# Optimization experiments

Measured on AMD Instinct MI355X. Metric: run time of the kernel, lower is better.

The kernel has to match this reference:

```python
import jax, jax.numpy as jnp
import numpy as np

FEAT_SIZE, HIDDEN_SIZE, ATT_SIZE = 2048, 1024, 512
BATCH, FEAT_NUM = 64, 512


def setup_inputs() -> dict:
    key = jax.random.key(0)
    ks = jax.random.split(key, 8)
    s = lambda fan_in: 1.0 / np.sqrt(fan_in)
    return {
        "feats": jax.random.normal(ks[0], (BATCH, FEAT_NUM, FEAT_SIZE), jnp.float32),
        "key": jax.random.normal(ks[1], (BATCH, HIDDEN_SIZE), jnp.float32),
        "wh_w": jax.random.uniform(ks[2], (ATT_SIZE, HIDDEN_SIZE), jnp.float32, -s(HIDDEN_SIZE), s(HIDDEN_SIZE)),
        "wh_b": jax.random.uniform(ks[3], (ATT_SIZE,), jnp.float32, -s(HIDDEN_SIZE), s(HIDDEN_SIZE)),
        "wv_w": jax.random.uniform(ks[4], (ATT_SIZE, FEAT_SIZE), jnp.float32, -s(FEAT_SIZE), s(FEAT_SIZE)),
        "wv_b": jax.random.uniform(ks[5], (ATT_SIZE,), jnp.float32, -s(FEAT_SIZE), s(FEAT_SIZE)),
        "wa_w": jax.random.uniform(ks[6], (1, ATT_SIZE), jnp.float32, -s(ATT_SIZE), s(ATT_SIZE)),
    }


def reference(feats, key, wh_w, wh_b, wv_w, wv_b, wa_w):
    # v = wv(feats): (B, N, A)
    v = jnp.einsum('bnf,af->bna', feats, wv_w) + wv_b
    # h = wh(key): (B, A), broadcast-added over feat_num
    h = key @ wh_w.T + wh_b
    inputs = h[:, None, :] + v                       # (B, N, A)
    scores = jnp.einsum('bna,a->bn', jnp.tanh(inputs), wa_w[0])  # (B, N)
    alpha = jax.nn.softmax(scores, axis=1)           # (B, N)
    att_feats = jnp.einsum('bn,bnf->bf', alpha, feats)  # (B, F)
    return (att_feats, alpha)
```

## Files before the change

kernel.cpp:

```cpp
#include <hip/hip_runtime.h>
#include <hip/hip_bf16.h>

#define FEATSZ 2048
#define HIDSZ  1024
#define ATTSZ  512
#define BATCH  64
#define FEATN  512

typedef float  f32x4  __attribute__((ext_vector_type(4)));
typedef __bf16 bf16x8 __attribute__((ext_vector_type(8)));

__device__ __forceinline__ unsigned short f2bf(float f) {
    union { float f; unsigned int u; } x; x.f = f;
    unsigned int u = x.u;
    return (unsigned short)((u + 0x7fffu + ((u >> 16) & 1u)) >> 16);
}

__global__ void k_h(const float* __restrict__ key, const float* __restrict__ wh_w,
                    const float* __restrict__ wh_b, float* __restrict__ h) {
    const int b = blockIdx.y;
    const int ac = blockIdx.x;
    const int t = threadIdx.x;
    const int lane = t & 63, wv = t >> 6;
    float k16[16];
    const float* kb = key + b * HIDSZ;
#pragma unroll
    for (int j = 0; j < 16; ++j) k16[j] = kb[lane + 64 * j];
#pragma unroll 1
    for (int i = 0; i < 16; ++i) {
        int a = ac * 64 + wv * 16 + i;
        const float* wr = wh_w + (size_t)a * HIDSZ;
        float s = 0.f;
#pragma unroll
        for (int j = 0; j < 16; ++j) s += k16[j] * wr[lane + 64 * j];
#pragma unroll
        for (int d = 32; d; d >>= 1) s += __shfl_xor(s, d);
        if (lane == 0) h[b * ATTSZ + a] = s + wh_b[a];
    }
}

__global__ void k_wvcvt(const float* __restrict__ wv_w, unsigned short* __restrict__ wvb) {
    int idx = blockIdx.x * 256 + threadIdx.x;
    int a = idx >> 11, k = idx & 2047;
    int CF = a >> 4, c = a & 15, ks = k >> 5, kin = k & 31;
    int lane = c + ((kin >> 3) << 4);
    int dst = ((ks * 32 + CF) * 64 + lane) * 8 + (kin & 7);
    wvb[dst] = f2bf(wv_w[idx]);
}

__global__ __launch_bounds__(256, 4) void k_scores(
        const float* __restrict__ feats, const unsigned short* __restrict__ wvb,
        const float* __restrict__ h, const float* __restrict__ wv_b,
        const float* __restrict__ wa, float* __restrict__ part_sc) {
    __shared__ __align__(16) char smem[40960];

    const int t = threadIdx.x, lane = t & 63, w = t >> 6;
    const int wm = w >> 1, wn = w & 1;
    const int xcd = blockIdx.x & 7, idx = blockIdx.x >> 3;
    const int mb = xcd * 32 + (idx >> 2);
    const int nc = idx & 3;
    const int m0 = mb * 128, b = mb >> 2;

    auto Abuf = [&](int i) -> char* { return smem + i * 8192; };
    auto Bbuf = [&](int i) -> char* { return smem + 16384 + i * 8192; };

    const int sr = t >> 1, shf = t & 1;
    const float* gA = feats + (size_t)(m0 + sr) * FEATSZ + shf * 16;
    const int sx = (sr >> 1) & 3;
    const int wof0 = sr * 64 + (((shf * 2    ) ^ sx) * 16);
    const int wof1 = sr * 64 + (((shf * 2 + 1) ^ sx) * 16);

    const char* gBb = (const char*)wvb + (size_t)(nc * 8) * 1024 + (size_t)(w * 2) * 1024 + lane * 16;
    const int bdst = (w * 2) * 1024;

    const int l15 = lane & 15;
    const int abase = (wm * 64 + l15) * 64 + (((lane >> 4) ^ ((l15 >> 1) & 3)) * 16);
    const int bbase = (wn * 4) * 1024 + lane * 16;

    f32x4 acc[4][4];
#pragma unroll
    for (int m = 0; m < 4; ++m)
#pragma unroll
        for (int cf = 0; cf < 4; ++cf) acc[m][cf] = (f32x4)0.0f;

    f32x4 GA0, GA1, GA2, GA3;

    auto gloadB = [&](char* dst, int kk) {
#pragma unroll
        for (int i = 0; i < 2; ++i)
            __builtin_amdgcn_global_load_lds(
                (const __attribute__((address_space(1))) void*)(gBb + (size_t)kk * 32768 + i * 1024),
                (__attribute__((address_space(3))) void*)(dst + bdst + i * 1024),
                16, 0, 0);
    };
    auto ldGA = [&](int kk) {
        const float* p = gA + kk * 32;
        GA0 = *(const f32x4*)p;       GA1 = *(const f32x4*)(p + 4);
        GA2 = *(const f32x4*)(p + 8); GA3 = *(const f32x4*)(p + 12);
    };
    auto cvtWrite = [&](char* dst) {
        bf16x8 v0, v1;
        v0[0] = (__bf16)GA0[0]; v0[1] = (__bf16)GA0[1]; v0[2] = (__bf16)GA0[2]; v0[3] = (__bf16)GA0[3];
        v0[4] = (__bf16)GA1[0]; v0[5] = (__bf16)GA1[1]; v0[6] = (__bf16)GA1[2]; v0[7] = (__bf16)GA1[3];
        v1[0] = (__bf16)GA2[0]; v1[1] = (__bf16)GA2[1]; v1[2] = (__bf16)GA2[2]; v1[3] = (__bf16)GA2[3];
        v1[4] = (__bf16)GA3[0]; v1[5] = (__bf16)GA3[1]; v1[6] = (__bf16)GA3[2]; v1[7] = (__bf16)GA3[3];
        *(bf16x8*)__builtin_assume_aligned(dst + wof0, 16) = v0;
        *(bf16x8*)__builtin_assume_aligned(dst + wof1, 16) = v1;
    };

    ldGA(0);
    gloadB(Bbuf(0), 0);
    gloadB(Bbuf(1), 1);
    cvtWrite(Abuf(0));
    ldGA(1);
    asm volatile("s_waitcnt vmcnt(6)" ::: "memory");
    asm volatile("s_waitcnt lgkmcnt(0)" ::: "memory");
    __builtin_amdgcn_s_barrier();
    __builtin_amdgcn_sched_barrier(0);

#pragma unroll 1
    for (int j = 0; j < 64; ++j) {
        const char* ar = Abuf(j & 1);
        char*       aw = Abuf((j & 1) ^ 1);
        const char* br = Bbuf(j % 3);
        if (j < 62) gloadB(Bbuf((j + 2) % 3), j + 2);
        bf16x8 BF[4], AF[4];
#pragma unroll
        for (int cf = 0; cf < 4; ++cf)
            BF[cf] = *(const bf16x8*)__builtin_assume_aligned(br + bbase + cf * 1024, 16);
#pragma unroll
        for (int m = 0; m < 4; ++m)
            AF[m] = *(const bf16x8*)__builtin_assume_aligned(ar + abase + m * 1024, 16);
        __builtin_amdgcn_s_setprio(1);
#pragma unroll
        for (int m = 0; m < 4; ++m)
#pragma unroll
            for (int cf = 0; cf < 4; ++cf)
                acc[m][cf] = __builtin_amdgcn_mfma_f32_16x16x32_bf16(AF[m], BF[cf], acc[m][cf], 0, 0, 0);
        __builtin_amdgcn_s_setprio(0);
        if (j < 63) cvtWrite(aw);
        if (j < 62) ldGA(j + 2);
        if (j < 62) asm volatile("s_waitcnt vmcnt(6)" ::: "memory");
        else        asm volatile("s_waitcnt vmcnt(0)" ::: "memory");
        asm volatile("s_waitcnt lgkmcnt(0)" ::: "memory");
        __builtin_amdgcn_s_barrier();
        __builtin_amdgcn_sched_barrier(0);
    }

    const int c16 = lane & 15, q4 = lane >> 4;
    float hreg[4], wreg[4];
#pragma unroll
    for (int cf = 0; cf < 4; ++cf) {
        int a = nc * 128 + wn * 64 + cf * 16 + c16;
        hreg[cf] = h[b * ATTSZ + a] + wv_b[a];
        wreg[cf] = wa[a];
    }
    float pv[4][4];
#pragma unroll
    for (int m = 0; m < 4; ++m)
#pragma unroll
        for (int jr = 0; jr < 4; ++jr) pv[m][jr] = 0.f;
#pragma unroll
    for (int m = 0; m < 4; ++m)
#pragma unroll
        for (int cf = 0; cf < 4; ++cf)
#pragma unroll
            for (int jr = 0; jr < 4; ++jr)
                pv[m][jr] += tanhf(acc[m][cf][jr] + hreg[cf]) * wreg[cf];
#pragma unroll
    for (int m = 0; m < 4; ++m)
#pragma unroll
        for (int jr = 0; jr < 4; ++jr) {
            float v = pv[m][jr];
            v += __shfl_xor(v, 1); v += __shfl_xor(v, 2);
            v += __shfl_xor(v, 4); v += __shfl_xor(v, 8);
            pv[m][jr] = v;
        }
    float* scp = (float*)smem;
    __builtin_amdgcn_s_barrier();
    if (c16 == 0) {
#pragma unroll
        for (int m = 0; m < 4; ++m)
#pragma unroll
            for (int jr = 0; jr < 4; ++jr)
                scp[wn * 128 + wm * 64 + m * 16 + q4 * 4 + jr] = pv[m][jr];
    }
    __syncthreads();
    if (t < 128)
        part_sc[(size_t)nc * (BATCH * FEATN) + m0 + t] = scp[t] + scp[128 + t];
}

__global__ void k_softmax(const float* __restrict__ part_sc, float* __restrict__ alpha) {
    __shared__ float red[16];
    const int b = blockIdx.x, t = threadIdx.x;
    const int lane = t & 63, w = t >> 6;
    const int r = b * FEATN + t;
    float s = part_sc[r] + part_sc[BATCH * FEATN + r]
            + part_sc[2 * BATCH * FEATN + r] + part_sc[3 * BATCH * FEATN + r];
    float m = s;
#pragma unroll
    for (int d = 32; d; d >>= 1) m = fmaxf(m, __shfl_xor(m, d));
    if (lane == 0) red[w] = m;
    __syncthreads();
    if (t == 0) {
        float mm = red[0];
        for (int i = 1; i < 8; ++i) mm = fmaxf(mm, red[i]);
        red[8] = mm;
    }
    __syncthreads();
    float e = __expf(s - red[8]);
    float sum = e;
#pragma unroll
    for (int d = 32; d; d >>= 1) sum += __shfl_xor(sum, d);
    if (lane == 0) red[w] = sum;
    __syncthreads();
    if (t == 0) {
        float ss = 0.f;
        for (int i = 0; i < 8; ++i) ss += red[i];
        red[9] = 1.0f / ss;
    }
    __syncthreads();
    alpha[b * FEATN + t] = e * red[9];
}

__global__ void k_att_part(const float* __restrict__ feats, const float* __restrict__ alpha,
                           float* __restrict__ part) {
    const int b = blockIdx.x, fc = blockIdx.y, ns = blockIdx.z, t = threadIdx.x;
    const int f0 = fc * 1024 + t * 4;
    const float* fp = feats + (size_t)(b * FEATN + ns * 128) * FEATSZ + f0;
    const float* al = alpha + b * FEATN + ns * 128;
    float4 acc = {0.f, 0.f, 0.f, 0.f};
#pragma unroll 4
    for (int i = 0; i < 128; ++i) {
        float a = al[i];
        float4 v = *(const float4*)(fp + (size_t)i * FEATSZ);
        acc.x += a * v.x; acc.y += a * v.y; acc.z += a * v.z; acc.w += a * v.w;
    }
    *(float4*)(part + ((size_t)ns * BATCH + b) * FEATSZ + f0) = acc;
}

__global__ void k_att_red(const float* __restrict__ part, float* __restrict__ out) {
    const int idx = (blockIdx.x * 256 + threadIdx.x) * 4;
    float4 s = *(const float4*)(part + idx);
#pragma unroll
    for (int z = 1; z < 4; ++z) {
        float4 v = *(const float4*)(part + (size_t)z * (BATCH * FEATSZ) + idx);
        s.x += v.x; s.y += v.y; s.z += v.z; s.w += v.w;
    }
    *(float4*)(out + idx) = s;
}

extern "C" void kernel_launch(void* const* d_in, const int* in_sizes, int n_in,
                              void* d_out, int out_size, void* d_ws, size_t ws_size,
                              hipStream_t stream) {
    const float* feats = (const float*)d_in[0];
    const float* key   = (const float*)d_in[1];
    const float* wh_w  = (const float*)d_in[2];
    const float* wh_b  = (const float*)d_in[3];
    const float* wv_w  = (const float*)d_in[4];
    const float* wv_b  = (const float*)d_in[5];
    const float* wa_w  = (const float*)d_in[6];

    float* out_att   = (float*)d_out;
    float* out_alpha = out_att + BATCH * FEATSZ;

    char* ws = (char*)d_ws;
    float* h            = (float*)(ws);
    float* part_sc      = (float*)(ws + 131072);
    unsigned short* wvb = (unsigned short*)(ws + 655360);
    float* part         = (float*)(ws + 655360);

    hipLaunchKernelGGL(k_h,        dim3(8, 64),    dim3(256), 0, stream, key, wh_w, wh_b, h);
    hipLaunchKernelGGL(k_wvcvt,    dim3(4096),     dim3(256), 0, stream, wv_w, wvb);
    hipLaunchKernelGGL(k_scores,   dim3(1024),     dim3(256), 0, stream, feats, wvb, h, wv_b, wa_w, part_sc);
    hipLaunchKernelGGL(k_softmax,  dim3(64),       dim3(512), 0, stream, part_sc, out_alpha);
    hipLaunchKernelGGL(k_att_part, dim3(64, 2, 4), dim3(256), 0, stream, feats, out_alpha, part);
    hipLaunchKernelGGL(k_att_red,  dim3(128),      dim3(256), 0, stream, part, out_att);
}
```

Measured before the change: 184.7 us.

## Double K-step per iteration in scores GEMM to halve barriers

The scores GEMM main loop now processes a K-chunk of 64 per iteration instead of 32, with two MFMA sub-steps per barrier. The feats staging loads 32 floats per thread, and the LDS swizzle is widened to 128-byte rows. Wv is double-buffered instead of triple-buffered, and LDS per block grows to 64KB with the occupancy hint removed. The aim is to halve the barrier and waitcnt count per unit of work, at the cost of fewer resident blocks per CU and a shallower B prefetch.

```diff
diff --git a/kernel.cpp b/kernel.cpp
--- a/kernel.cpp
+++ b/kernel.cpp
@@ -48,11 +48,11 @@
     wvb[dst] = f2bf(wv_w[idx]);
 }
 
-__global__ __launch_bounds__(256, 4) void k_scores(
+__global__ __launch_bounds__(256) void k_scores(
         const float* __restrict__ feats, const unsigned short* __restrict__ wvb,
         const float* __restrict__ h, const float* __restrict__ wv_b,
         const float* __restrict__ wa, float* __restrict__ part_sc) {
-    __shared__ __align__(16) char smem[40960];
+    __shared__ __align__(16) char smem[65536];
 
     const int t = threadIdx.x, lane = t & 63, w = t >> 6;
     const int wm = w >> 1, wn = w & 1;
@@ -61,20 +61,27 @@
     const int nc = idx & 3;
     const int m0 = mb * 128, b = mb >> 2;
 
-    auto Abuf = [&](int i) -> char* { return smem + i * 8192; };
-    auto Bbuf = [&](int i) -> char* { return smem + 16384 + i * 8192; };
+    auto Abuf = [&](int i) -> char* { return smem + i * 16384; };
+    auto Bbuf = [&](int i) -> char* { return smem + 32768 + i * 16384; };
 
     const int sr = t >> 1, shf = t & 1;
-    const float* gA = feats + (size_t)(m0 + sr) * FEATSZ + shf * 16;
-    const int sx = (sr >> 1) & 3;
-    const int wof0 = sr * 64 + (((shf * 2    ) ^ sx) * 16);
-    const int wof1 = sr * 64 + (((shf * 2 + 1) ^ sx) * 16);
-
-    const char* gBb = (const char*)wvb + (size_t)(nc * 8) * 1024 + (size_t)(w * 2) * 1024 + lane * 16;
-    const int bdst = (w * 2) * 1024;
-
-    const int l15 = lane & 15;
-    const int abase = (wm * 64 + l15) * 64 + (((lane >> 4) ^ ((l15 >> 1) & 3)) * 16);
+    const float* gA = feats + (size_t)(m0 + sr) * FEATSZ + shf * 32;
+    int wof[4];
+#pragma unroll
+    for (int q = 0; q < 4; ++q)
+        wof[q] = sr * 128 + (((shf * 4 + q) ^ (sr & 7)) * 16);
+
+    const char* wvbb = (const char*)wvb;
+    unsigned int bsrc[4];
+#pragma unroll
+    for (int i = 0; i < 4; ++i) {
+        int c = w * 4 + i;
+        bsrc[i] = (unsigned int)(((c >> 3) * 32 + nc * 8 + (c & 7)) * 1024 + lane * 16);
+    }
+    const int bdst0 = (w * 4) * 1024 + lane * 16;
+
+    const int l15 = lane & 15, aq = lane >> 4, ax = lane & 7;
+    const int arow = (wm * 64 + l15) * 128;
     const int bbase = (wn * 4) * 1024 + lane * 16;
 
     f32x4 acc[4][4];
@@ -83,65 +90,76 @@
 #pragma unroll
         for (int cf = 0; cf < 4; ++cf) acc[m][cf] = (f32x4)0.0f;
 
-    f32x4 GA0, GA1, GA2, GA3;
-
-    auto gloadB = [&](char* dst, int kk) {
-#pragma unroll
-        for (int i = 0; i < 2; ++i)
+    f32x4 GA0, GA1, GA2, GA3, GA4, GA5, GA6, GA7;
+
+    auto gloadB = [&](char* dst, int j) {
+#pragma unroll
+        for (int i = 0; i < 4; ++i)
             __builtin_amdgcn_global_load_lds(
-                (const __attribute__((address_space(1))) void*)(gBb + (size_t)kk * 32768 + i * 1024),
-                (__attribute__((address_space(3))) void*)(dst + bdst + i * 1024),
+                (const __attribute__((address_space(1))) void*)(wvbb + (size_t)j * 65536 + bsrc[i]),
+                (__attribute__((address_space(3))) void*)(dst + bdst0 + i * 1024),
                 16, 0, 0);
     };
-    auto ldGA = [&](int kk) {
-        const float* p = gA + kk * 32;
-        GA0 = *(const f32x4*)p;       GA1 = *(const f32x4*)(p + 4);
-        GA2 = *(const f32x4*)(p + 8); GA3 = *(const f32x4*)(p + 12);
+    auto ldGA = [&](int j) {
+        const float* p = gA + j * 64;
+        GA0 = *(const f32x4*)(p);      GA1 = *(const f32x4*)(p + 4);
+        GA2 = *(const f32x4*)(p + 8);  GA3 = *(const f32x4*)(p + 12);
+        GA4 = *(const f32x4*)(p + 16); GA5 = *(const f32x4*)(p + 20);
+        GA6 = *(const f32x4*)(p + 24); GA7 = *(const f32x4*)(p + 28);
     };
     auto cvtWrite = [&](char* dst) {
-        bf16x8 v0, v1;
-        v0[0] = (__bf16)GA0[0]; v0[1] = (__bf16)GA0[1]; v0[2] = (__bf16)GA0[2]; v0[3] = (__bf16)GA0[3];
-        v0[4] = (__bf16)GA1[0]; v0[5] = (__bf16)GA1[1]; v0[6] = (__bf16)GA1[2]; v0[7] = (__bf16)GA1[3];
-        v1[0] = (__bf16)GA2[0]; v1[1] = (__bf16)GA2[1]; v1[2] = (__bf16)GA2[2]; v1[3] = (__bf16)GA2[3];
-        v1[4] = (__bf16)GA3[0]; v1[5] = (__bf16)GA3[1]; v1[6] = (__bf16)GA3[2]; v1[7] = (__bf16)GA3[3];
-        *(bf16x8*)__builtin_assume_aligned(dst + wof0, 16) = v0;
-        *(bf16x8*)__builtin_assume_aligned(dst + wof1, 16) = v1;
+        bf16x8 v0, v1, v2, v3;
+        v0[0]=(__bf16)GA0[0]; v0[1]=(__bf16)GA0[1]; v0[2]=(__bf16)GA0[2]; v0[3]=(__bf16)GA0[3];
+        v0[4]=(__bf16)GA1[0]; v0[5]=(__bf16)GA1[1]; v0[6]=(__bf16)GA1[2]; v0[7]=(__bf16)GA1[3];
+        v1[0]=(__bf16)GA2[0]; v1[1]=(__bf16)GA2[1]; v1[2]=(__bf16)GA2[2]; v1[3]=(__bf16)GA2[3];
+        v1[4]=(__bf16)GA3[0]; v1[5]=(__bf16)GA3[1]; v1[6]=(__bf16)GA3[2]; v1[7]=(__bf16)GA3[3];
+        v2[0]=(__bf16)GA4[0]; v2[1]=(__bf16)GA4[1]; v2[2]=(__bf16)GA4[2]; v2[3]=(__bf16)GA4[3];
+        v2[4]=(__bf16)GA5[0]; v2[5]=(__bf16)GA5[1]; v2[6]=(__bf16)GA5[2]; v2[7]=(__bf16)GA5[3];
+        v3[0]=(__bf16)GA6[0]; v3[1]=(__bf16)GA6[1]; v3[2]=(__bf16)GA6[2]; v3[3]=(__bf16)GA6[3];
+        v3[4]=(__bf16)GA7[0]; v3[5]=(__bf16)GA7[1]; v3[6]=(__bf16)GA7[2]; v3[7]=(__bf16)GA7[3];
+        *(bf16x8*)__builtin_assume_aligned(dst + wof[0], 16) = v0;
+        *(bf16x8*)__builtin_assume_aligned(dst + wof[1], 16) = v1;
+        *(bf16x8*)__builtin_assume_aligned(dst + wof[2], 16) = v2;
+        *(bf16x8*)__builtin_assume_aligned(dst + wof[3], 16) = v3;
     };
 
     ldGA(0);
     gloadB(Bbuf(0), 0);
-    gloadB(Bbuf(1), 1);
     cvtWrite(Abuf(0));
     ldGA(1);
-    asm volatile("s_waitcnt vmcnt(6)" ::: "memory");
+    asm volatile("s_waitcnt vmcnt(8)" ::: "memory");
     asm volatile("s_waitcnt lgkmcnt(0)" ::: "memory");
     __builtin_amdgcn_s_barrier();
     __builtin_amdgcn_sched_barrier(0);
 
 #pragma unroll 1
-    for (int j = 0; j < 64; ++j) {
+    for (int j = 0; j < 32; ++j) {
         const char* ar = Abuf(j & 1);
         char*       aw = Abuf((j & 1) ^ 1);
-        const char* br = Bbuf(j % 3);
-        if (j < 62) gloadB(Bbuf((j + 2) % 3), j + 2);
-        bf16x8 BF[4], AF[4];
-#pragma unroll
-        for (int cf = 0; cf < 4; ++cf)
-            BF[cf] = *(const bf16x8*)__builtin_assume_aligned(br + bbase + cf * 1024, 16);
-#pragma unroll
-        for (int m = 0; m < 4; ++m)
-            AF[m] = *(const bf16x8*)__builtin_assume_aligned(ar + abase + m * 1024, 16);
-        __builtin_amdgcn_s_setprio(1);
-#pragma unroll
-        for (int m = 0; m < 4; ++m)
+        const char* br = Bbuf(j & 1);
+        char*       bw = Bbuf((j & 1) ^ 1);
+        if (j < 31) gloadB(bw, j + 1);
+#pragma unroll
+        for (int ks = 0; ks < 2; ++ks) {
+            bf16x8 BF[4], AF[4];
 #pragma unroll
             for (int cf = 0; cf < 4; ++cf)
-                acc[m][cf] = __builtin_amdgcn_mfma_f32_16x16x32_bf16(AF[m], BF[cf], acc[m][cf], 0, 0, 0);
-        __builtin_amdgcn_s_setprio(0);
-        if (j < 63) cvtWrite(aw);
-        if (j < 62) ldGA(j + 2);
-        if (j < 62) asm volatile("s_waitcnt vmcnt(6)" ::: "memory");
-        else        asm volatile("s_waitcnt vmcnt(0)" ::: "memory");
+                BF[cf] = *(const bf16x8*)__builtin_assume_aligned(br + (ks * 8) * 1024 + bbase + cf * 1024, 16);
+#pragma unroll
+            for (int m = 0; m < 4; ++m)
+                AF[m] = *(const bf16x8*)__builtin_assume_aligned(ar + arow + m * 2048 + (((ks * 4 + aq) ^ ax) * 16), 16);
+            __builtin_amdgcn_s_setprio(1);
+#pragma unroll
+            for (int m = 0; m < 4; ++m)
+#pragma unroll
+                for (int cf = 0; cf < 4; ++cf)
+                    acc[m][cf] = __builtin_amdgcn_mfma_f32_16x16x32_bf16(AF[m], BF[cf], acc[m][cf], 0, 0, 0);
+            __builtin_amdgcn_s_setprio(0);
+        }
+        if (j < 31) cvtWrite(aw);
+        if (j < 30) ldGA(j + 2);
+        if (j < 30)      asm volatile("s_waitcnt vmcnt(8)" ::: "memory");
+        else             asm volatile("s_waitcnt vmcnt(0)" ::: "memory");
         asm volatile("s_waitcnt lgkmcnt(0)" ::: "memory");
         __builtin_amdgcn_s_barrier();
         __builtin_amdgcn_sched_barrier(0);
```

Result: slower. 225.5 us (+22.1%).
